# Kernel tuning notes

Measured on AMD Instinct MI355X. Metric: run time of the kernel, lower is better.

Reference implementation:

```python
import jax, jax.numpy as jnp
import numpy as np

D_MODEL = 512
NUM_HEADS = 8
D_K = D_MODEL // NUM_HEADS


def setup_inputs() -> dict:
    key = jax.random.key(0)
    ks = jax.random.split(key, 12)
    B, Sq, Sk = 4, 2048, 2048
    scale = 1.0 / np.sqrt(D_MODEL)
    inp = {
        'query': jax.random.normal(ks[0], (B, Sq, D_MODEL), jnp.float32),
        'key':   jax.random.normal(ks[1], (B, Sk, D_MODEL), jnp.float32),
        'value': jax.random.normal(ks[2], (B, Sk, D_MODEL), jnp.float32),
        'wq': jax.random.normal(ks[3], (D_MODEL, D_MODEL), jnp.float32) * scale,
        'bq': jnp.zeros((D_MODEL,), jnp.float32),
        'wk': jax.random.normal(ks[4], (D_MODEL, D_MODEL), jnp.float32) * scale,
        'bk': jnp.zeros((D_MODEL,), jnp.float32),
        'wv': jax.random.normal(ks[5], (D_MODEL, D_MODEL), jnp.float32) * scale,
        'bv': jnp.zeros((D_MODEL,), jnp.float32),
        'wo': jax.random.normal(ks[6], (D_MODEL, D_MODEL), jnp.float32) * scale,
        'bo': jnp.zeros((D_MODEL,), jnp.float32),
        'ln_g': jnp.ones((D_MODEL,), jnp.float32),
        'ln_b': jnp.zeros((D_MODEL,), jnp.float32),
    }
    return inp


def _layer_norm(x, g, b, eps=1e-5):
    mu = jnp.mean(x, axis=-1, keepdims=True)
    var = jnp.mean(jnp.square(x - mu), axis=-1, keepdims=True)
    return (x - mu) * jax.lax.rsqrt(var + eps) * g + b


def reference(query, key, value, wq, bq, wk, bk, wv, bv, wo, bo, ln_g, ln_b):
    B, Sq, _ = query.shape
    Sk = key.shape[1]
    residual = query
    # projections: torch Linear computes x @ W^T + b; here wq is (out,in)-free:
    # we store weights as (d_model, d_model) and use x @ W + b (equivalent param space)
    Q = (query @ wq + bq).reshape(B, Sq, NUM_HEADS, D_K).transpose(0, 2, 1, 3)
    K = (key   @ wk + bk).reshape(B, Sk, NUM_HEADS, D_K).transpose(0, 2, 1, 3)
    V = (value @ wv + bv).reshape(B, Sk, NUM_HEADS, D_K).transpose(0, 2, 1, 3)
    scores = jnp.einsum('bhqd,bhkd->bhqk', Q, K) / jnp.sqrt(jnp.float32(D_K))
    attn = jax.nn.softmax(scores, axis=-1)  # dropout is identity in eval
    context = jnp.einsum('bhqk,bhkd->bhqd', attn, V)
    context = context.transpose(0, 2, 1, 3).reshape(B, Sq, D_MODEL)
    out = context @ wo + bo
    return _layer_norm(out + residual, ln_g, ln_b)
```

## Files before the change

kernel.cpp:

```cpp
#include <hip/hip_runtime.h>
#include <cstdint>
#include <cstddef>

typedef unsigned short u16;
typedef __bf16 bf16x8 __attribute__((ext_vector_type(8)));
typedef __bf16 bf16x4 __attribute__((ext_vector_type(4)));
typedef float f32x4 __attribute__((ext_vector_type(4)));

#define DEVI __device__ __forceinline__

DEVI u16 f2bf(float f){
  union { float f; unsigned u; } v; v.f = f;
  unsigned r = v.u + 0x7fffu + ((v.u >> 16) & 1u);
  return (u16)(r >> 16);
}

#if defined(__has_builtin)
#if __has_builtin(__builtin_amdgcn_exp2f)
#define EXP2F(x) __builtin_amdgcn_exp2f(x)
#else
#define EXP2F(x) exp2f(x)
#endif
#else
#define EXP2F(x) exp2f(x)
#endif

#define MFMA16(a,b,c) __builtin_amdgcn_mfma_f32_16x16x32_bf16((a),(b),(c),0,0,0)

DEVI void gload_lds16(const void* g, void* l){
  __builtin_amdgcn_global_load_lds(
      (const __attribute__((address_space(1))) void*)g,
      (__attribute__((address_space(3))) void*)l, 16, 0, 0);
}

#define PIPE_SYNC do{ asm volatile("s_waitcnt vmcnt(0)" ::: "memory"); \
    __builtin_amdgcn_s_barrier(); \
    __builtin_amdgcn_sched_barrier(0); }while(0)

#define PIPE_SYNC_VL do{ asm volatile("s_waitcnt vmcnt(0) lgkmcnt(0)" ::: "memory"); \
    __builtin_amdgcn_s_barrier(); \
    __builtin_amdgcn_sched_barrier(0); }while(0)


__global__ void k_prep_x(const float* __restrict__ q, const float* __restrict__ k,
                         const float* __restrict__ v, u16* __restrict__ xb){
  size_t t = (size_t)blockIdx.x*blockDim.x + threadIdx.x;
  size_t base = t*8;
  const float* s;
  if (base < 4194304u)      s = q + base;
  else if (base < 8388608u) s = k + (base - 4194304u);
  else                      s = v + (base - 8388608u);
  float4 a = *(const float4*)s;
  float4 b = *(const float4*)(s+4);
  ushort4 o0, o1;
  o0.x=f2bf(a.x); o0.y=f2bf(a.y); o0.z=f2bf(a.z); o0.w=f2bf(a.w);
  o1.x=f2bf(b.x); o1.y=f2bf(b.y); o1.z=f2bf(b.z); o1.w=f2bf(b.w);
  *(ushort4*)(xb + base)     = o0;
  *(ushort4*)(xb + base + 4) = o1;
}

__global__ void k_prep_w(const float* __restrict__ w0, const float* __restrict__ w1,
                         const float* __restrict__ w2, const float* __restrict__ w3,
                         u16* __restrict__ wt){
  __shared__ u16 tile[64][72];
  int p = blockIdx.z;
  const float* W = (p==0)?w0:((p==1)?w1:((p==2)?w2:w3));
  int k0 = blockIdx.x*64, n0 = blockIdx.y*64;
  int t = threadIdx.x;
  int tr = t >> 4, tc = t & 15;
  #pragma unroll
  for (int pass=0; pass<4; pass++){
    int row = pass*16 + tr;
    float4 a = *(const float4*)(W + (size_t)(k0+row)*512 + n0 + tc*4);
    tile[row][tc*4+0] = f2bf(a.x);
    tile[row][tc*4+1] = f2bf(a.y);
    tile[row][tc*4+2] = f2bf(a.z);
    tile[row][tc*4+3] = f2bf(a.w);
  }
  __syncthreads();
  #pragma unroll
  for (int pass=0; pass<4; pass++){
    int n = pass*16 + tr;
    ushort4 o;
    o.x = tile[tc*4+0][n];
    o.y = tile[tc*4+1][n];
    o.z = tile[tc*4+2][n];
    o.w = tile[tc*4+3][n];
    *(ushort4*)(wt + (size_t)p*262144 + (size_t)(n0+n)*512 + k0 + tc*4) = o;
  }
}

__global__ __launch_bounds__(256)
void k_gemm_qkv(const u16* __restrict__ xb, const u16* __restrict__ wt,
                const float* __restrict__ bq, const float* __restrict__ bk,
                const float* __restrict__ bv,
                u16* __restrict__ qb, u16* __restrict__ kb, u16* __restrict__ vt){
  int l = threadIdx.x & 63, w = threadIdx.x >> 6;
  int lr = l & 15, lg = l >> 4;
  int f = blockIdx.x;
  int xcd = f & 7, j0 = f >> 3;
  int pm   = xcd*24 + (j0 >> 2);
  int nblk = j0 & 3;
  int p    = pm >> 6, mblk = pm & 63;
  int wr = w >> 1, wc = w & 1;

  const float* bias = (p==0)?bq:((p==1)?bk:bv);
  float osc = (p==0)? (0.125f*1.44269504088896340736f) : 1.0f;

  const char* Ag = (const char*)(xb + (size_t)p*4194304 + (size_t)mblk*128*512);
  const char* Bg = (const char*)(wt + (size_t)p*262144  + (size_t)nblk*128*512);

  __shared__ __align__(16) u16 Albuf[2][8192];
  __shared__ __align__(16) u16 Blbuf[2][8192];

  int r8 = l >> 3, sl = l & 7;

  #define STAGE_G(t, buf) do{ \
    _Pragma("unroll") \
    for (int cc=0; cc<4; ++cc){ \
      int c = w*4 + cc; int row = c*8 + r8; \
      int sw = (sl ^ (row & 7)) << 4; \
      gload_lds16(Ag + (size_t)row*1024 + (size_t)(t)*128 + sw, (char*)Albuf[buf] + c*1024); \
      gload_lds16(Bg + (size_t)row*1024 + (size_t)(t)*128 + sw, (char*)Blbuf[buf] + c*1024); \
    } }while(0)

  STAGE_G(0, 0);
  PIPE_SYNC;

  f32x4 acc[4][4] = {};
  for (int t = 0; t < 8; ++t){
    int cur = t & 1;
    if (t < 7) STAGE_G(t+1, cur^1);
    const char* Ac = (const char*)Albuf[cur];
    const char* Bc = (const char*)Blbuf[cur];
    #pragma unroll
    for (int kk=0;kk<2;kk++){
      int ks = ((kk*4 + lg) ^ (lr & 7)) << 4;
      bf16x8 af[4], bfr[4];
      #pragma unroll
      for (int i=0;i<4;i++)
        af[i]  = *(const bf16x8*)(Ac + (wr*64 + i*16 + lr)*128 + ks);
      #pragma unroll
      for (int j=0;j<4;j++)
        bfr[j] = *(const bf16x8*)(Bc + (wc*64 + j*16 + lr)*128 + ks);
      #pragma unroll
      for (int i=0;i<4;i++)
        #pragma unroll
        for (int j=0;j<4;j++)
          acc[i][j] = MFMA16(af[i], bfr[j], acc[i][j]);
    }
    if (t < 7) PIPE_SYNC;
  }
  #undef STAGE_G

  int m0 = mblk*128 + wr*64;
  int n0 = nblk*128 + wc*64;
  if (p < 2){
    u16* outp = (p==0)?qb:kb;
    #pragma unroll
    for (int i=0;i<4;i++){
      #pragma unroll
      for (int j=0;j<4;j++){
        int n = n0 + j*16 + lr;
        int h = n >> 6, d = n & 63;
        float bb = bias[n];
        #pragma unroll
        for (int rg=0;rg<4;rg++){
          int m = m0 + i*16 + 4*lg + rg;
          int b = m >> 11, s = m & 2047;
          float val = (acc[i][j][rg] + bb)*osc;
          __bf16 hb = (__bf16)val;
          outp[(((size_t)b*8 + h)*2048 + s)*64 + d] = *(u16*)&hb;
        }
      }
    }
  } else {
    #pragma unroll
    for (int i=0;i<4;i++){
      #pragma unroll
      for (int j=0;j<4;j++){
        int n = n0 + j*16 + lr;
        int h = n >> 6, d = n & 63;
        float bb = bias[n];
        int m = m0 + i*16 + 4*lg;
        int b = m >> 11, s = m & 2047;
        ushort4 o;
        #pragma unroll
        for (int rg=0;rg<4;rg++){
          __bf16 hb = (__bf16)(acc[i][j][rg] + bb);
          ((u16*)&o)[rg] = *(u16*)&hb;
        }
        *(ushort4*)(vt + (((size_t)(b*8+h)*64 + d)*2048 + s)) = o;
      }
    }
  }
}

__global__ __launch_bounds__(512, 4)
void k_attn(const u16* __restrict__ qbuf, const u16* __restrict__ kbuf,
            const u16* __restrict__ vtb, u16* __restrict__ opart,
            float* __restrict__ lpart){
  int l = threadIdx.x & 63, w = threadIdx.x >> 6;
  int lr = l & 15, lg = l >> 4;
  int f = blockIdx.x;
  int bh    = (f & 7)*4 + ((f >> 3) & 3);
  int rest  = f >> 5;
  int split = rest & 1;
  int q0    = (rest >> 1)*256 + w*32;
  int b = bh >> 3, h = bh & 7;
  int kvbase = split*1024;

  const u16* Qp = qbuf + ((size_t)bh*2048 + q0)*64;
  const char* Kg = (const char*)(kbuf + (size_t)bh*2048*64) + (size_t)kvbase*128;
  const char* Vg = (const char*)(vtb  + (size_t)bh*64*2048) + (size_t)kvbase*2;

  __shared__ __align__(16) u16 Klds[2][4096];
  __shared__ __align__(16) u16 Vlds[2][4096];
  __shared__ __align__(16) u16 Plds[8][2048];
  u16* Pw = Plds[w];

  int r8 = l >> 3, sl = l & 7;

  bf16x8 qf[2][2];
  #pragma unroll
  for (int j=0;j<2;j++)
    #pragma unroll
    for (int kk=0;kk<2;kk++)
      qf[j][kk] = *(const bf16x8*)(Qp + (size_t)(j*16+lr)*64 + kk*32 + lg*8);

  {
    int row = w*8 + r8;
    int sw = (sl ^ (row & 7)) << 4;
    gload_lds16(Kg + (size_t)row*128 + sw,  (char*)Klds[0] + w*1024);
    gload_lds16(Vg + (size_t)row*4096 + sw, (char*)Vlds[0] + w*1024);
  }
  PIPE_SYNC;

  f32x4 oacc[2][4] = {};
  float lsum[2] = {0.f, 0.f};
  const float M = 16.0f;

  for (int t = 0; t < 16; ++t){
    int cur = t & 1;
    if (t < 15){
      int row = w*8 + r8;
      int sw = (sl ^ (row & 7)) << 4;
      gload_lds16(Kg + (size_t)(t+1)*8192 + (size_t)row*128 + sw,
                  (char*)Klds[cur^1] + w*1024);
      gload_lds16(Vg + (size_t)(t+1)*128 + (size_t)row*4096 + sw,
                  (char*)Vlds[cur^1] + w*1024);
    }
    const char* Kc = (const char*)Klds[cur];
    const char* Vc = (const char*)Vlds[cur];
    f32x4 sacc[4][2] = {};
    #pragma unroll
    for (int kk=0;kk<2;kk++){
      bf16x8 kf[4];
      #pragma unroll
      for (int i=0;i<4;i++)
        kf[i] = *(const bf16x8*)(Kc + (i*16+lr)*128 + (((4*kk+lg)^(lr&7))<<4));
      __builtin_amdgcn_s_setprio(1);
      #pragma unroll
      for (int i=0;i<4;i++)
        #pragma unroll
        for (int j=0;j<2;j++)
          sacc[i][j] = MFMA16(kf[i], qf[j][kk], sacc[i][j]);
      __builtin_amdgcn_s_setprio(0);
    }
    #pragma unroll
    for (int j=0;j<2;j++){
      int qrow = lr + 16*j;
      #pragma unroll
      for (int i=0;i<4;i++){
        bf16x4 pk;
        #pragma unroll
        for (int rg=0;rg<4;rg++){
          float pv = EXP2F(sacc[i][j][rg] - M);
          lsum[j] += pv;
          pk[rg] = (__bf16)pv;
        }
        int o    = 8*lg + 32*i;
        int slot = (o >> 4) ^ (qrow & 7);
        *(bf16x4*)((char*)Pw + qrow*128 + (slot<<4) + (o & 15)) = pk;
      }
    }
    #pragma unroll
    for (int kk=0;kk<2;kk++){
      bf16x8 pf[2];
      #pragma unroll
      for (int fi=0;fi<2;fi++){
        int qrow = fi*16 + lr;
        int slot = (4*kk + lg) ^ (qrow & 7);
        pf[fi] = *(const bf16x8*)((char*)Pw + qrow*128 + (slot<<4));
      }
      bf16x8 vf[4];
      #pragma unroll
      for (int fj=0;fj<4;fj++)
        vf[fj] = *(const bf16x8*)(Vc + (fj*16+lr)*128 + (((4*kk+lg)^(lr&7))<<4));
      __builtin_amdgcn_s_setprio(1);
      #pragma unroll
      for (int fi=0;fi<2;fi++)
        #pragma unroll
        for (int fj=0;fj<4;fj++)
          oacc[fi][fj] = MFMA16(pf[fi], vf[fj], oacc[fi][fj]);
      __builtin_amdgcn_s_setprio(0);
    }
    if (t < 15) PIPE_SYNC;
  }

  #pragma unroll
  for (int j=0;j<2;j++){
    lsum[j] += __shfl_xor(lsum[j], 16);
    lsum[j] += __shfl_xor(lsum[j], 32);
  }
  if (lg == 0){
    #pragma unroll
    for (int j=0;j<2;j++)
      lpart[((size_t)split*32 + bh)*2048 + q0 + 16*j + lr] = lsum[j];
  }
  u16* op = opart + (size_t)split*8192*512;
  #pragma unroll
  for (int fi=0;fi<2;fi++){
    #pragma unroll
    for (int fj=0;fj<4;fj++){
      int col = h*64 + fj*16 + lr;
      #pragma unroll
      for (int rg=0;rg<4;rg++){
        int qg = q0 + fi*16 + 4*lg + rg;
        __bf16 hb = (__bf16)oacc[fi][fj][rg];
        op[((size_t)(b*2048 + qg))*512 + col] = *(u16*)&hb;
      }
    }
  }
}

__global__ __launch_bounds__(256)
void k_gemm_o(const u16* __restrict__ op0, const u16* __restrict__ op1,
              const float* __restrict__ lpart, const u16* __restrict__ wto,
              u16* __restrict__ gout){
  int l = threadIdx.x & 63, w = threadIdx.x >> 6;
  int lr = l & 15, lg = l >> 4;
  int f = blockIdx.x;
  int xcd = f & 7, j0 = f >> 3;
  int mblk = xcd*16 + (j0 >> 2);
  int nblk = j0 & 3;
  int wr = w & 1, wc = w >> 1;

  int bb8 = (mblk >> 5) * 8;
  int qbase = (mblk & 31) * 64;

  const u16* Ag0 = op0 + (size_t)mblk*64*512;
  const u16* Ag1 = op1 + (size_t)mblk*64*512;
  const char* Bg = (const char*)(wto + (size_t)nblk*128*512);

  __shared__ __align__(16) u16 Albuf[2][4096];
  __shared__ __align__(16) u16 Blbuf[2][8192];

  int r8 = l >> 3, sl = l & 7;

  bf16x8 a0v[2], a1v[2]; float l0v[2], l1v[2];
  #define A_ISSUE(tt) do{ \
    _Pragma("unroll") \
    for (int cc=0; cc<2; ++cc){ \
      int c = w*2 + cc; int row = c*8 + r8; \
      int ssrc = sl ^ (row & 7); \
      a0v[cc] = *(const bf16x8*)(Ag0 + (size_t)row*512 + (tt)*64 + ssrc*8); \
      a1v[cc] = *(const bf16x8*)(Ag1 + (size_t)row*512 + (tt)*64 + ssrc*8); \
      int q = qbase + row; \
      l0v[cc] = lpart[(size_t)(bb8 + (tt))*2048 + q]; \
      l1v[cc] = lpart[(size_t)(32 + bb8 + (tt))*2048 + q]; \
    } }while(0)

  #define A_WRITE(buf) do{ \
    _Pragma("unroll") \
    for (int cc=0; cc<2; ++cc){ \
      int c = w*2 + cc; \
      float inv = 1.f / (l0v[cc] + l1v[cc]); \
      bf16x8 r; \
      _Pragma("unroll") \
      for (int e=0;e<8;e++) \
        r[e] = (__bf16)(((float)a0v[cc][e] + (float)a1v[cc][e]) * inv); \
      *(bf16x8*)((char*)Albuf[buf] + c*1024 + r8*128 + sl*16) = r; \
    } }while(0)

  #define B_STAGE(tt, buf) do{ \
    _Pragma("unroll") \
    for (int cc=0; cc<4; ++cc){ \
      int c = w*4 + cc; int row = c*8 + r8; \
      int sw = (sl ^ (row & 7)) << 4; \
      gload_lds16(Bg + (size_t)row*1024 + (size_t)(tt)*128 + sw, (char*)Blbuf[buf] + c*1024); \
    } }while(0)

  A_ISSUE(0);
  B_STAGE(0, 0);
  asm volatile("s_waitcnt vmcnt(0)" ::: "memory");
  A_WRITE(0);
  PIPE_SYNC_VL;

  f32x4 acc[2][4] = {};
  for (int t = 0; t < 8; ++t){
    int cur = t & 1;
    if (t < 7){ A_ISSUE(t+1); B_STAGE(t+1, cur^1); }
    const char* Ac = (const char*)Albuf[cur];
    const char* Bc = (const char*)Blbuf[cur];
    #pragma unroll
    for (int kk=0;kk<2;kk++){
      int ks = ((kk*4 + lg) ^ (lr & 7)) << 4;
      bf16x8 af[2], bfr[4];
      #pragma unroll
      for (int i=0;i<2;i++)
        af[i]  = *(const bf16x8*)(Ac + (wr*32 + i*16 + lr)*128 + ks);
      #pragma unroll
      for (int j=0;j<4;j++)
        bfr[j] = *(const bf16x8*)(Bc + (wc*64 + j*16 + lr)*128 + ks);
      __builtin_amdgcn_s_setprio(1);
      #pragma unroll
      for (int i=0;i<2;i++)
        #pragma unroll
        for (int j=0;j<4;j++)
          acc[i][j] = MFMA16(af[i], bfr[j], acc[i][j]);
      __builtin_amdgcn_s_setprio(0);
    }
    if (t < 7){
      asm volatile("s_waitcnt vmcnt(0)" ::: "memory");
      A_WRITE(cur^1);
      PIPE_SYNC_VL;
    }
  }
  #undef A_ISSUE
  #undef A_WRITE
  #undef B_STAGE

  int m0 = mblk*64 + wr*32;
  int n0 = nblk*128 + wc*64;
  #pragma unroll
  for (int i=0;i<2;i++){
    #pragma unroll
    for (int j=0;j<4;j++){
      int n = n0 + j*16 + lr;
      #pragma unroll
      for (int rg=0;rg<4;rg++){
        int m = m0 + i*16 + 4*lg + rg;
        __bf16 hb = (__bf16)acc[i][j][rg];
        gout[(size_t)m*512 + n] = *(u16*)&hb;
      }
    }
  }
}

__global__ __launch_bounds__(256)
void k_ln(const u16* __restrict__ gout, const float* __restrict__ bo,
          const float* __restrict__ resid, const float* __restrict__ g,
          const float* __restrict__ beta, float* __restrict__ out){
  int gid  = blockIdx.x*256 + threadIdx.x;
  int row  = gid >> 6;
  int lane = gid & 63;
  int c0 = lane*8;
  bf16x8 a = *(const bf16x8*)(gout + (size_t)row*512 + c0);
  float4 r0 = *(const float4*)(resid + (size_t)row*512 + c0);
  float4 r1 = *(const float4*)(resid + (size_t)row*512 + c0 + 4);
  float4 b0 = *(const float4*)(bo + c0);
  float4 b1 = *(const float4*)(bo + c0 + 4);
  float v[8];
  v[0]=(float)a[0]+b0.x+r0.x; v[1]=(float)a[1]+b0.y+r0.y;
  v[2]=(float)a[2]+b0.z+r0.z; v[3]=(float)a[3]+b0.w+r0.w;
  v[4]=(float)a[4]+b1.x+r1.x; v[5]=(float)a[5]+b1.y+r1.y;
  v[6]=(float)a[6]+b1.z+r1.z; v[7]=(float)a[7]+b1.w+r1.w;
  float s1 = 0.f, s2 = 0.f;
  #pragma unroll
  for (int e=0;e<8;e++){ s1 += v[e]; s2 += v[e]*v[e]; }
  #pragma unroll
  for (int mk=1; mk<64; mk<<=1){
    s1 += __shfl_xor(s1, mk);
    s2 += __shfl_xor(s2, mk);
  }
  float mu   = s1 * (1.f/512.f);
  float var  = s2 * (1.f/512.f) - mu*mu;
  float rstd = rsqrtf(var + 1e-5f);
  float4 g0 = *(const float4*)(g + c0);
  float4 g1 = *(const float4*)(g + c0 + 4);
  float4 e0 = *(const float4*)(beta + c0);
  float4 e1 = *(const float4*)(beta + c0 + 4);
  float4 o0, o1;
  o0.x=(v[0]-mu)*rstd*g0.x+e0.x; o0.y=(v[1]-mu)*rstd*g0.y+e0.y;
  o0.z=(v[2]-mu)*rstd*g0.z+e0.z; o0.w=(v[3]-mu)*rstd*g0.w+e0.w;
  o1.x=(v[4]-mu)*rstd*g1.x+e1.x; o1.y=(v[5]-mu)*rstd*g1.y+e1.y;
  o1.z=(v[6]-mu)*rstd*g1.z+e1.z; o1.w=(v[7]-mu)*rstd*g1.w+e1.w;
  *(float4*)(out + (size_t)row*512 + c0)     = o0;
  *(float4*)(out + (size_t)row*512 + c0 + 4) = o1;
}

extern "C" void kernel_launch(void* const* d_in, const int* in_sizes, int n_in,
                              void* d_out, int out_size, void* d_ws, size_t ws_size,
                              hipStream_t stream){
  const float* q   = (const float*)d_in[0];
  const float* k   = (const float*)d_in[1];
  const float* v   = (const float*)d_in[2];
  const float* wq  = (const float*)d_in[3];
  const float* bq  = (const float*)d_in[4];
  const float* wk  = (const float*)d_in[5];
  const float* bk  = (const float*)d_in[6];
  const float* wv  = (const float*)d_in[7];
  const float* bv  = (const float*)d_in[8];
  const float* wo  = (const float*)d_in[9];
  const float* bo  = (const float*)d_in[10];
  const float* lng = (const float*)d_in[11];
  const float* lnb = (const float*)d_in[12];
  float* out = (float*)d_out;
  char* ws = (char*)d_ws;
  u16*   xb    = (u16*)(ws + 0);
  u16*   opart = (u16*)(ws + 0);
  float* lpart = (float*)(ws + 16777216);
  u16*   wt    = (u16*)(ws + 25165824);
  u16*   qb    = (u16*)(ws + 27262976);
  u16*   kb    = (u16*)(ws + 35651584);
  u16*   vt    = (u16*)(ws + 44040192);
  u16*   gout  = (u16*)(ws + 52428800);

  k_prep_x<<<6144, 256, 0, stream>>>(q, k, v, xb);
  k_prep_w<<<dim3(8,8,4), 256, 0, stream>>>(wq, wk, wv, wo, wt);
  k_gemm_qkv<<<768, 256, 0, stream>>>(xb, wt, bq, bk, bv, qb, kb, vt);
  k_attn<<<512, 512, 0, stream>>>(qb, kb, vt, opart, lpart);
  k_gemm_o<<<512, 256, 0, stream>>>(opart, opart + (size_t)8192*512, lpart,
                                    wt + 3*262144, gout);
  k_ln<<<2048, 256, 0, stream>>>(gout, bo, q, lng, lnb, out);
}
```

Measured before the change: 105.3 us.

## Use partial vmcnt waits to overlap next-tile loads with compute

New measurement: 102.7 us. 1.03x faster.

```diff
diff --git a/kernel.cpp b/kernel.cpp
--- a/kernel.cpp
+++ b/kernel.cpp
@@ -33,12 +33,7 @@
       (__attribute__((address_space(3))) void*)l, 16, 0, 0);
 }
 
-#define PIPE_SYNC do{ asm volatile("s_waitcnt vmcnt(0)" ::: "memory"); \
-    __builtin_amdgcn_s_barrier(); \
-    __builtin_amdgcn_sched_barrier(0); }while(0)
-
-#define PIPE_SYNC_VL do{ asm volatile("s_waitcnt vmcnt(0) lgkmcnt(0)" ::: "memory"); \
-    __builtin_amdgcn_s_barrier(); \
+#define BARRIER do{ __builtin_amdgcn_s_barrier(); \
     __builtin_amdgcn_sched_barrier(0); }while(0)
 
 
@@ -125,12 +120,17 @@
     } }while(0)
 
   STAGE_G(0, 0);
-  PIPE_SYNC;
 
   f32x4 acc[4][4] = {};
   for (int t = 0; t < 8; ++t){
     int cur = t & 1;
-    if (t < 7) STAGE_G(t+1, cur^1);
+    if (t < 7){
+      STAGE_G(t+1, cur^1);
+      asm volatile("s_waitcnt vmcnt(8)" ::: "memory");
+    } else {
+      asm volatile("s_waitcnt vmcnt(0)" ::: "memory");
+    }
+    BARRIER;
     const char* Ac = (const char*)Albuf[cur];
     const char* Bc = (const char*)Blbuf[cur];
     #pragma unroll
@@ -149,7 +149,7 @@
         for (int j=0;j<4;j++)
           acc[i][j] = MFMA16(af[i], bfr[j], acc[i][j]);
     }
-    if (t < 7) PIPE_SYNC;
+    if (t < 7) BARRIER;
   }
   #undef STAGE_G
 
@@ -234,7 +234,6 @@
     gload_lds16(Kg + (size_t)row*128 + sw,  (char*)Klds[0] + w*1024);
     gload_lds16(Vg + (size_t)row*4096 + sw, (char*)Vlds[0] + w*1024);
   }
-  PIPE_SYNC;
 
   f32x4 oacc[2][4] = {};
   float lsum[2] = {0.f, 0.f};
@@ -249,7 +248,11 @@
                   (char*)Klds[cur^1] + w*1024);
       gload_lds16(Vg + (size_t)(t+1)*128 + (size_t)row*4096 + sw,
                   (char*)Vlds[cur^1] + w*1024);
-    }
+      asm volatile("s_waitcnt vmcnt(2)" ::: "memory");
+    } else {
+      asm volatile("s_waitcnt vmcnt(0)" ::: "memory");
+    }
+    BARRIER;
     const char* Kc = (const char*)Klds[cur];
     const char* Vc = (const char*)Vlds[cur];
     f32x4 sacc[4][2] = {};
@@ -259,13 +262,11 @@
       #pragma unroll
       for (int i=0;i<4;i++)
         kf[i] = *(const bf16x8*)(Kc + (i*16+lr)*128 + (((4*kk+lg)^(lr&7))<<4));
-      __builtin_amdgcn_s_setprio(1);
       #pragma unroll
       for (int i=0;i<4;i++)
         #pragma unroll
         for (int j=0;j<2;j++)
           sacc[i][j] = MFMA16(kf[i], qf[j][kk], sacc[i][j]);
-      __builtin_amdgcn_s_setprio(0);
     }
     #pragma unroll
     for (int j=0;j<2;j++){
@@ -297,15 +298,13 @@
       #pragma unroll
       for (int fj=0;fj<4;fj++)
         vf[fj] = *(const bf16x8*)(Vc + (fj*16+lr)*128 + (((4*kk+lg)^(lr&7))<<4));
-      __builtin_amdgcn_s_setprio(1);
       #pragma unroll
       for (int fi=0;fi<2;fi++)
         #pragma unroll
         for (int fj=0;fj<4;fj++)
           oacc[fi][fj] = MFMA16(pf[fi], vf[fj], oacc[fi][fj]);
-      __builtin_amdgcn_s_setprio(0);
-    }
-    if (t < 15) PIPE_SYNC;
+    }
+    if (t < 15) BARRIER;
   }
 
   #pragma unroll
@@ -393,14 +392,21 @@
 
   A_ISSUE(0);
   B_STAGE(0, 0);
-  asm volatile("s_waitcnt vmcnt(0)" ::: "memory");
+  asm volatile("s_waitcnt vmcnt(4)" ::: "memory");
   A_WRITE(0);
-  PIPE_SYNC_VL;
+  asm volatile("s_waitcnt lgkmcnt(0)" ::: "memory");
 
   f32x4 acc[2][4] = {};
   for (int t = 0; t < 8; ++t){
     int cur = t & 1;
-    if (t < 7){ A_ISSUE(t+1); B_STAGE(t+1, cur^1); }
+    if (t < 7){
+      A_ISSUE(t+1);
+      B_STAGE(t+1, cur^1);
+      asm volatile("s_waitcnt vmcnt(12)" ::: "memory");
+    } else {
+      asm volatile("s_waitcnt vmcnt(0)" ::: "memory");
+    }
+    BARRIER;
     const char* Ac = (const char*)Albuf[cur];
     const char* Bc = (const char*)Blbuf[cur];
     #pragma unroll
@@ -413,18 +419,17 @@
       #pragma unroll
       for (int j=0;j<4;j++)
         bfr[j] = *(const bf16x8*)(Bc + (wc*64 + j*16 + lr)*128 + ks);
-      __builtin_amdgcn_s_setprio(1);
       #pragma unroll
       for (int i=0;i<2;i++)
         #pragma unroll
         for (int j=0;j<4;j++)
           acc[i][j] = MFMA16(af[i], bfr[j], acc[i][j]);
-      __builtin_amdgcn_s_setprio(0);
     }
     if (t < 7){
-      asm volatile("s_waitcnt vmcnt(0)" ::: "memory");
+      asm volatile("s_waitcnt vmcnt(4)" ::: "memory");
       A_WRITE(cur^1);
-      PIPE_SYNC_VL;
+      asm volatile("s_waitcnt lgkmcnt(0)" ::: "memory");
+      BARRIER;
     }
   }
   #undef A_ISSUE
```
